# Kernel tuning notes

Hardware: AMD Instinct MI355X
Metric: run time of the kernel (lower is better)

Reference implementation:

```python
import jax, jax.numpy as jnp
import numpy as np

B2 = 8192  # 2 * batch (two SimCLR views)
D = 512    # feature_dim


def setup_inputs() -> dict:
    key = jax.random.key(0)
    k1, k2, k3 = jax.random.split(key, 3)
    feature = jax.random.normal(k1, (B2, D), dtype=jnp.float32)
    # sigma (diagonal variances) must be strictly positive: uniform in [0.5, 1.5]
    sigma_v = jax.random.uniform(k2, (B2, D), dtype=jnp.float32, minval=0.5, maxval=1.5)
    # label indexes the (B2-1) skip-self columns -> values in [0, B2-2]
    label = jax.random.randint(k3, (B2,), 0, B2 - 1)
    return {"feature": feature, "sigma_v": sigma_v, "label": label}


def reference(feature, sigma_v, label):
    n, d = feature.shape
    rows = jnp.arange(n)
    cols = jnp.arange(n - 1)
    # gather_index[b, k] = k if k < b else k + 1  (all indices except b)
    gi = cols[None, :] + (cols[None, :] >= rows[:, None]).astype(jnp.int32)  # (B2, B2-1)

    inv_s = 1.0 / sigma_v
    # weighted Mahalanobis: dist[i, j] = sum_d (x_i - x_j)^2 / sigma_j, expanded to GEMMs
    t1 = (feature * feature) @ inv_s.T                 # sum_d x_i^2 / sigma_j
    t2 = feature @ (feature * inv_s).T                 # sum_d x_i x_j / sigma_j
    t3 = jnp.sum(feature * feature * inv_s, axis=1)    # sum_d x_j^2 / sigma_j
    dist = t1 - 2.0 * t2 + t3[None, :]                 # (B2, B2)

    dist_g = jnp.take_along_axis(dist, gi, axis=1)               # (B2, B2-1)
    gt = jnp.take_along_axis(dist_g, label[:, None], axis=1)     # (B2, 1)
    logit = jnp.exp(0.1 * (gt - dist_g))                         # (B2, B2-1)

    # absolute index of each row's positive sample
    pos_idx = jnp.take_along_axis(gi, label[:, None], axis=1)[:, 0]  # (B2,)
    # ratio[i, j] = prod_d sqrt(sigma_i[d] / sigma_pos(j)[d]) = exp(0.5 * (ls[i] - ls[pos(j)]))
    ls = jnp.sum(jnp.log(sigma_v), axis=1)                           # (B2,)
    ratio_g = jnp.exp(0.5 * (ls[:, None] - ls[pos_idx][gi]))         # (B2, B2-1)

    logit_mat = ratio_g * logit
    loss = jnp.mean(jnp.log(jnp.sum(logit_mat, axis=1)))
    return loss, logit_mat
```

## Files before the change

kernel.cpp:

```cpp
#include <hip/hip_runtime.h>
#include <hip/hip_bf16.h>
#include <stdint.h>

#define B2 8192
#define D  512
#define K2 1024
#define NM1 (B2 - 1)

typedef _Float16 f16;
typedef _Float16 f16x2 __attribute__((ext_vector_type(2)));
typedef _Float16 f16x8 __attribute__((ext_vector_type(8)));
typedef float    f32x4 __attribute__((ext_vector_type(4)));

__global__ __launch_bounds__(256) void prep(
    const float* __restrict__ feat, const float* __restrict__ sig,
    const int* __restrict__ label,
    f16* __restrict__ Ahat, f16* __restrict__ Bhat,
    float* __restrict__ rowc, float* __restrict__ colc2, float* __restrict__ rowsum)
{
    int i = blockIdx.x;
    int t = threadIdx.x;
    int lb = label[i];
    int p  = lb + (lb >= i ? 1 : 0);

    const float2 xv  = ((const float2*)(feat + (size_t)i * D))[t];
    const float2 sv  = ((const float2*)(sig  + (size_t)i * D))[t];
    const float2 xpv = ((const float2*)(feat + (size_t)p * D))[t];
    const float2 spv = ((const float2*)(sig  + (size_t)p * D))[t];

    float inv0 = 1.0f / sv.x, inv1 = 1.0f / sv.y;
    float x20 = xv.x * xv.x, x21 = xv.y * xv.y;

    f16* Ar = Ahat + (size_t)i * K2;
    f16* Br = Bhat + (size_t)i * K2;
    *(f16x2*)&Ar[2 * t]       = f16x2{(f16)x20, (f16)x21};
    *(f16x2*)&Ar[512 + 2 * t] = f16x2{(f16)xv.x, (f16)xv.y};
    *(f16x2*)&Br[2 * t]       = f16x2{(f16)inv0, (f16)inv1};
    *(f16x2*)&Br[512 + 2 * t] = f16x2{(f16)(-2.0f * xv.x * inv0), (f16)(-2.0f * xv.y * inv1)};

    float t3p = x20 * inv0 + x21 * inv1;
    float lsp = __logf(sv.x) + __logf(sv.y);
    float lpp = __logf(spv.x) + __logf(spv.y);
    float dx0 = xv.x - xpv.x, dx1 = xv.y - xpv.y;
    float gtp = dx0 * dx0 / spv.x + dx1 * dx1 / spv.y;

    for (int off = 32; off; off >>= 1) {
        t3p += __shfl_down(t3p, off);
        lsp += __shfl_down(lsp, off);
        lpp += __shfl_down(lpp, off);
        gtp += __shfl_down(gtp, off);
    }
    __shared__ float w0[4], w1[4], w2[4], w3[4];
    int lane = t & 63, w = t >> 6;
    if (lane == 0) { w0[w] = t3p; w1[w] = lsp; w2[w] = lpp; w3[w] = gtp; }
    __syncthreads();
    if (t == 0) {
        float t3 = w0[0] + w0[1] + w0[2] + w0[3];
        float ls = w1[0] + w1[1] + w1[2] + w1[3];
        float lp = w2[0] + w2[1] + w2[2] + w2[3];
        float gt = w3[0] + w3[1] + w3[2] + w3[3];
        rowc[i]  = 0.1f * gt + 0.5f * ls;
        colc2[i] = -0.5f * lp - 0.1f * t3;
        rowsum[i] = 0.0f;
    }
}

__global__ __launch_bounds__(256, 4) void gemm_epilogue(
    const f16* __restrict__ Ahat, const f16* __restrict__ Bhat,
    const float* __restrict__ rowc, const float* __restrict__ colc2,
    float* __restrict__ rowsum, float* __restrict__ out)
{
    __shared__ f16 As[128 * 64];
    __shared__ f16 Bs[128 * 64];
    __shared__ float rS[128], cS[128];

    int bid = blockIdx.x;
    int bn = ((bid >> 9) << 3) + (bid & 7);
    int bm = (bid >> 3) & 63;

    int t = threadIdx.x;
    int l = t & 63, w = t >> 6;
    int wm = (w & 1) * 64, wn = (w >> 1) * 64;

    int srow   = t >> 3;
    int schunk = t & 7;
    int gchunk = schunk ^ (srow & 7);
    const f16* gA = Ahat + (size_t)(bm * 128 + srow) * K2 + gchunk * 8;
    const f16* gB = Bhat + (size_t)(bn * 128 + srow) * K2 + gchunk * 8;

    f32x4 zero4 = {0.f, 0.f, 0.f, 0.f};
    f32x4 acc[4][4];
    #pragma unroll
    for (int a = 0; a < 4; ++a)
        #pragma unroll
        for (int b = 0; b < 4; ++b) acc[a][b] = zero4;

    for (int kb = 0; kb < K2; kb += 64) {
        __syncthreads();
        #pragma unroll
        for (int rd = 0; rd < 4; ++rd) {
            __builtin_amdgcn_global_load_lds(
                (const __attribute__((address_space(1))) unsigned int*)(gA + (size_t)rd * 32 * K2 + kb),
                (__attribute__((address_space(3))) unsigned int*)(&As[rd * 2048 + w * 512]),
                16, 0, 0);
            __builtin_amdgcn_global_load_lds(
                (const __attribute__((address_space(1))) unsigned int*)(gB + (size_t)rd * 32 * K2 + kb),
                (__attribute__((address_space(3))) unsigned int*)(&Bs[rd * 2048 + w * 512]),
                16, 0, 0);
        }
        __syncthreads();

        #pragma unroll
        for (int ks = 0; ks < 2; ++ks) {
            f16x8 af[4], bf[4];
            int cl = (ks * 4 + (l >> 4)) ^ (l & 7);
            #pragma unroll
            for (int mi = 0; mi < 4; ++mi) {
                int ra = wm + mi * 16 + (l & 15);
                af[mi] = *(const f16x8*)&As[ra * 64 + cl * 8];
                int rb = wn + mi * 16 + (l & 15);
                bf[mi] = *(const f16x8*)&Bs[rb * 64 + cl * 8];
            }
            #pragma unroll
            for (int mi = 0; mi < 4; ++mi)
                #pragma unroll
                for (int ni = 0; ni < 4; ++ni)
                    acc[mi][ni] = __builtin_amdgcn_mfma_f32_16x16x32_f16(
                        af[mi], bf[ni], acc[mi][ni], 0, 0, 0);
        }
    }

    if (t < 128)      rS[t]       = rowc[bm * 128 + t];
    else              cS[t - 128] = colc2[bn * 128 + (t - 128)];
    __syncthreads();

    int quad = l >> 4, lc = l & 15;
    #pragma unroll
    for (int mi = 0; mi < 4; ++mi) {
        #pragma unroll
        for (int rg = 0; rg < 4; ++rg) {
            int il = wm + mi * 16 + quad * 4 + rg;
            int i  = bm * 128 + il;
            float rc = rS[il];
            float part = 0.f;
            #pragma unroll
            for (int ni = 0; ni < 4; ++ni) {
                int jl = wn + ni * 16 + lc;
                int j  = bn * 128 + jl;
                float v = __expf(rc - 0.1f * acc[mi][ni][rg] + cS[jl]);
                if (j != i) {
                    out[1 + (size_t)i * NM1 + (j - (j > i ? 1 : 0))] = v;
                    part += v;
                }
            }
            part += __shfl_xor(part, 1);
            part += __shfl_xor(part, 2);
            part += __shfl_xor(part, 4);
            part += __shfl_xor(part, 8);
            if (lc == 0) atomicAdd(&rowsum[i], part);
        }
    }
}

__global__ __launch_bounds__(256) void loss_k(const float* __restrict__ rowsum,
                                              float* __restrict__ out)
{
    int t = threadIdx.x;
    float s = 0.f;
    for (int r = t; r < B2; r += 256) s += __logf(rowsum[r]);
    for (int off = 32; off; off >>= 1) s += __shfl_down(s, off);
    __shared__ float wv[4];
    if ((t & 63) == 0) wv[t >> 6] = s;
    __syncthreads();
    if (t == 0) out[0] = (wv[0] + wv[1] + wv[2] + wv[3]) * (1.0f / (float)B2);
}

extern "C" void kernel_launch(void* const* d_in, const int* in_sizes, int n_in,
                              void* d_out, int out_size, void* d_ws, size_t ws_size,
                              hipStream_t stream) {
    const float* feat  = (const float*)d_in[0];
    const float* sig   = (const float*)d_in[1];
    const int*   label = (const int*)d_in[2];
    float* out = (float*)d_out;

    char* ws = (char*)d_ws;
    f16* Ahat = (f16*)ws;
    f16* Bhat = (f16*)(ws + (size_t)B2 * K2 * 2);
    float* rowc   = (float*)(ws + (size_t)B2 * K2 * 4);
    float* colc2  = rowc + B2;
    float* rowsum = colc2 + B2;

    prep<<<dim3(B2), dim3(256), 0, stream>>>(feat, sig, label, Ahat, Bhat, rowc, colc2, rowsum);
    gemm_epilogue<<<dim3(4096), dim3(256), 0, stream>>>(Ahat, Bhat, rowc, colc2, rowsum, out);
    loss_k<<<dim3(1), dim3(256), 0, stream>>>(rowsum, out);
}
```

Baseline: 526.6 us.

## Use 256x256 tiles with double-buffered LDS and interleaved async loads in GEMM

Replaces the 128x128, 256-thread GEMM tile with a 256x256 tile run by 512 threads (8 waves) that double-buffers A and B in LDS. Global-to-LDS loads for the next k-slice are issued between MFMA phases, guarded by explicit barriers, waitcnt and setprio, so memory traffic overlaps compute. Block-to-tile mapping is also changed for L2 locality. This cuts operand re-reads and sync stalls, but the kernel now needs 128KB+ of LDS and one block per CU, which lowers occupancy, and the hand-written schedule is fragile.

```diff
diff --git a/kernel.cpp b/kernel.cpp
--- a/kernel.cpp
+++ b/kernel.cpp
@@ -6,6 +6,7 @@
 #define D  512
 #define K2 1024
 #define NM1 (B2 - 1)
+#define NT  16
 
 typedef _Float16 f16;
 typedef _Float16 f16x2 __attribute__((ext_vector_type(2)));
@@ -65,88 +66,202 @@
     }
 }
 
-__global__ __launch_bounds__(256, 4) void gemm_epilogue(
+
+#define GLDS16(src, dst)                                                       \
+  __builtin_amdgcn_global_load_lds(                                            \
+      (const __attribute__((address_space(1))) unsigned int*)(src),            \
+      (__attribute__((address_space(3))) unsigned int*)(dst), 16, 0, 0)
+
+#define STAGE_HALF(gbase, hrow, koff, dstbase)                                 \
+  do {                                                                         \
+    GLDS16((gbase) + (size_t)(hrow) * K2 + (koff), (dstbase) + w512);          \
+    GLDS16((gbase) + (size_t)((hrow) + 64) * K2 + (koff),                      \
+           (dstbase) + 4096 + w512);                                           \
+  } while (0)
+
+template <int VM>
+__device__ __forceinline__ void kquad(
+    const f16* Asb, const f16* Bsb,
+    f16* AsN,
+    f16* BsC,
+    const f16* gA, const f16* gB, int w512,
+    int doA, int kA, int doB, int kB,
+    int wr128, int wc64, int l15, int lhi, int l7,
+    f32x4 (&acc)[8][4])
+{
+    f16x8 bf[4][2], af[2][2];
+
+    #pragma unroll
+    for (int ni = 0; ni < 4; ++ni)
+        #pragma unroll
+        for (int ks = 0; ks < 2; ++ks)
+            bf[ni][ks] = *(const f16x8*)&Bsb[(wc64 + ni * 16 + l15) * 64 +
+                                             (((ks * 4 + lhi) ^ l7) * 8)];
+    #pragma unroll
+    for (int m = 0; m < 2; ++m)
+        #pragma unroll
+        for (int ks = 0; ks < 2; ++ks)
+            af[m][ks] = *(const f16x8*)&Asb[(wr128 + m * 16 + l15) * 64 +
+                                            (((ks * 4 + lhi) ^ l7) * 8)];
+    if (doA) { STAGE_HALF(gA, 0, kA, AsN); }
+    asm volatile("" ::: "memory");
+    __builtin_amdgcn_s_barrier();
+    asm volatile("s_waitcnt lgkmcnt(0)" ::: "memory");
+    __builtin_amdgcn_sched_barrier(0);
+    __builtin_amdgcn_s_setprio(1);
+    #pragma unroll
+    for (int m = 0; m < 2; ++m)
+        #pragma unroll
+        for (int ni = 0; ni < 4; ++ni)
+            #pragma unroll
+            for (int ks = 0; ks < 2; ++ks)
+                acc[m][ni] = __builtin_amdgcn_mfma_f32_16x16x32_f16(
+                    af[m][ks], bf[ni][ks], acc[m][ni], 0, 0, 0);
+    __builtin_amdgcn_s_setprio(0);
+    __builtin_amdgcn_s_barrier();
+
+    #pragma unroll
+    for (int m = 0; m < 2; ++m)
+        #pragma unroll
+        for (int ks = 0; ks < 2; ++ks)
+            af[m][ks] = *(const f16x8*)&Asb[(wr128 + (2 + m) * 16 + l15) * 64 +
+                                            (((ks * 4 + lhi) ^ l7) * 8)];
+    if (doA) { STAGE_HALF(gA, 128, kA, AsN + 8192); }
+    asm volatile("" ::: "memory");
+    if (doB) { STAGE_HALF(gB, 0, kB, BsC); }
+    asm volatile("" ::: "memory");
+    __builtin_amdgcn_s_barrier();
+    asm volatile("s_waitcnt lgkmcnt(0)" ::: "memory");
+    __builtin_amdgcn_sched_barrier(0);
+    __builtin_amdgcn_s_setprio(1);
+    #pragma unroll
+    for (int m = 0; m < 2; ++m)
+        #pragma unroll
+        for (int ni = 0; ni < 4; ++ni)
+            #pragma unroll
+            for (int ks = 0; ks < 2; ++ks)
+                acc[2 + m][ni] = __builtin_amdgcn_mfma_f32_16x16x32_f16(
+                    af[m][ks], bf[ni][ks], acc[2 + m][ni], 0, 0, 0);
+    __builtin_amdgcn_s_setprio(0);
+    __builtin_amdgcn_s_barrier();
+
+    #pragma unroll
+    for (int m = 0; m < 2; ++m)
+        #pragma unroll
+        for (int ks = 0; ks < 2; ++ks)
+            af[m][ks] = *(const f16x8*)&Asb[(wr128 + (4 + m) * 16 + l15) * 64 +
+                                            (((ks * 4 + lhi) ^ l7) * 8)];
+    if (doB) { STAGE_HALF(gB, 128, kB, BsC + 8192); }
+    asm volatile("" ::: "memory");
+    __builtin_amdgcn_s_barrier();
+    asm volatile("s_waitcnt lgkmcnt(0)" ::: "memory");
+    __builtin_amdgcn_sched_barrier(0);
+    __builtin_amdgcn_s_setprio(1);
+    #pragma unroll
+    for (int m = 0; m < 2; ++m)
+        #pragma unroll
+        for (int ni = 0; ni < 4; ++ni)
+            #pragma unroll
+            for (int ks = 0; ks < 2; ++ks)
+                acc[4 + m][ni] = __builtin_amdgcn_mfma_f32_16x16x32_f16(
+                    af[m][ks], bf[ni][ks], acc[4 + m][ni], 0, 0, 0);
+    __builtin_amdgcn_s_setprio(0);
+    __builtin_amdgcn_s_barrier();
+
+    #pragma unroll
+    for (int m = 0; m < 2; ++m)
+        #pragma unroll
+        for (int ks = 0; ks < 2; ++ks)
+            af[m][ks] = *(const f16x8*)&Asb[(wr128 + (6 + m) * 16 + l15) * 64 +
+                                            (((ks * 4 + lhi) ^ l7) * 8)];
+    __builtin_amdgcn_s_barrier();
+    asm volatile("s_waitcnt lgkmcnt(0)" ::: "memory");
+    __builtin_amdgcn_sched_barrier(0);
+    __builtin_amdgcn_s_setprio(1);
+    #pragma unroll
+    for (int m = 0; m < 2; ++m)
+        #pragma unroll
+        for (int ni = 0; ni < 4; ++ni)
+            #pragma unroll
+            for (int ks = 0; ks < 2; ++ks)
+                acc[6 + m][ni] = __builtin_amdgcn_mfma_f32_16x16x32_f16(
+                    af[m][ks], bf[ni][ks], acc[6 + m][ni], 0, 0, 0);
+    __builtin_amdgcn_s_setprio(0);
+    if (VM == 4) asm volatile("s_waitcnt vmcnt(4)" ::: "memory");
+    else         asm volatile("s_waitcnt vmcnt(0)" ::: "memory");
+    __builtin_amdgcn_s_barrier();
+}
+
+__global__ __launch_bounds__(512, 1) void gemm_epilogue(
     const f16* __restrict__ Ahat, const f16* __restrict__ Bhat,
     const float* __restrict__ rowc, const float* __restrict__ colc2,
     float* __restrict__ rowsum, float* __restrict__ out)
 {
-    __shared__ f16 As[128 * 64];
-    __shared__ f16 Bs[128 * 64];
-    __shared__ float rS[128], cS[128];
+    __shared__ f16 As[2][256 * 64];
+    __shared__ f16 Bs[2][256 * 64];
+    __shared__ float rS[256], cS[256];
 
     int bid = blockIdx.x;
-    int bn = ((bid >> 9) << 3) + (bid & 7);
-    int bm = (bid >> 3) & 63;
+    int rr = bid >> 3, x = bid & 7;
+    int bm = x * 4 + (rr & 3);
+    int bn = rr >> 2;
 
     int t = threadIdx.x;
     int l = t & 63, w = t >> 6;
-    int wm = (w & 1) * 64, wn = (w >> 1) * 64;
-
-    int srow   = t >> 3;
-    int schunk = t & 7;
-    int gchunk = schunk ^ (srow & 7);
-    const f16* gA = Ahat + (size_t)(bm * 128 + srow) * K2 + gchunk * 8;
-    const f16* gB = Bhat + (size_t)(bn * 128 + srow) * K2 + gchunk * 8;
-
-    f32x4 zero4 = {0.f, 0.f, 0.f, 0.f};
-    f32x4 acc[4][4];
-    #pragma unroll
-    for (int a = 0; a < 4; ++a)
-        #pragma unroll
-        for (int b = 0; b < 4; ++b) acc[a][b] = zero4;
-
-    for (int kb = 0; kb < K2; kb += 64) {
-        __syncthreads();
-        #pragma unroll
-        for (int rd = 0; rd < 4; ++rd) {
-            __builtin_amdgcn_global_load_lds(
-                (const __attribute__((address_space(1))) unsigned int*)(gA + (size_t)rd * 32 * K2 + kb),
-                (__attribute__((address_space(3))) unsigned int*)(&As[rd * 2048 + w * 512]),
-                16, 0, 0);
-            __builtin_amdgcn_global_load_lds(
-                (const __attribute__((address_space(1))) unsigned int*)(gB + (size_t)rd * 32 * K2 + kb),
-                (__attribute__((address_space(3))) unsigned int*)(&Bs[rd * 2048 + w * 512]),
-                16, 0, 0);
-        }
-        __syncthreads();
-
-        #pragma unroll
-        for (int ks = 0; ks < 2; ++ks) {
-            f16x8 af[4], bf[4];
-            int cl = (ks * 4 + (l >> 4)) ^ (l & 7);
-            #pragma unroll
-            for (int mi = 0; mi < 4; ++mi) {
-                int ra = wm + mi * 16 + (l & 15);
-                af[mi] = *(const f16x8*)&As[ra * 64 + cl * 8];
-                int rb = wn + mi * 16 + (l & 15);
-                bf[mi] = *(const f16x8*)&Bs[rb * 64 + cl * 8];
-            }
-            #pragma unroll
-            for (int mi = 0; mi < 4; ++mi)
-                #pragma unroll
-                for (int ni = 0; ni < 4; ++ni)
-                    acc[mi][ni] = __builtin_amdgcn_mfma_f32_16x16x32_f16(
-                        af[mi], bf[ni], acc[mi][ni], 0, 0, 0);
-        }
+    int wr128 = (w >> 2) * 128;
+    int wc64  = (w & 3) * 64;
+    int l15 = l & 15, lhi = l >> 4, l7 = l & 7;
+    int w512 = w * 512;
+
+    int gcs = (t & 7) ^ ((t >> 3) & 7);
+    const f16* gA = Ahat + (size_t)(bm * 256 + (t >> 3)) * K2 + gcs * 8;
+    const f16* gB = Bhat + (size_t)(bn * 256 + (t >> 3)) * K2 + gcs * 8;
+
+    if (t < 256) rS[t]       = rowc[bm * 256 + t];
+    else         cS[t - 256] = colc2[bn * 256 + (t - 256)];
+
+    STAGE_HALF(gA, 0,   0,  &As[0][0]);
+    STAGE_HALF(gA, 128, 0,  &As[0][8192]);
+    STAGE_HALF(gB, 0,   0,  &Bs[0][0]);
+    STAGE_HALF(gB, 128, 0,  &Bs[0][8192]);
+    STAGE_HALF(gB, 0,   64, &Bs[1][0]);
+    STAGE_HALF(gB, 128, 64, &Bs[1][8192]);
+    __syncthreads();
+
+    f32x4 acc[8][4];
+    #pragma unroll
+    for (int a = 0; a < 8; ++a)
+        #pragma unroll
+        for (int b = 0; b < 4; ++b) acc[a][b] = f32x4{0.f, 0.f, 0.f, 0.f};
+
+    #pragma unroll 1
+    for (int it = 0; it < 7; ++it) {
+        int T = 2 * it;
+        kquad<4>(&As[0][0], &Bs[0][0], &As[1][0], &Bs[0][0], gA, gB, w512,
+                 1, (T + 1) * 64, 1, (T + 2) * 64,
+                 wr128, wc64, l15, lhi, l7, acc);
+        kquad<4>(&As[1][0], &Bs[1][0], &As[0][0], &Bs[1][0], gA, gB, w512,
+                 1, (T + 2) * 64, 1, (T + 3) * 64,
+                 wr128, wc64, l15, lhi, l7, acc);
     }
-
-    if (t < 128)      rS[t]       = rowc[bm * 128 + t];
-    else              cS[t - 128] = colc2[bn * 128 + (t - 128)];
-    __syncthreads();
-
-    int quad = l >> 4, lc = l & 15;
-    #pragma unroll
-    for (int mi = 0; mi < 4; ++mi) {
+    kquad<0>(&As[0][0], &Bs[0][0], &As[1][0], &Bs[0][0], gA, gB, w512,
+             1, 15 * 64, 0, 0, wr128, wc64, l15, lhi, l7, acc);
+    kquad<0>(&As[1][0], &Bs[1][0], &As[0][0], &Bs[1][0], gA, gB, w512,
+             0, 0, 0, 0, wr128, wc64, l15, lhi, l7, acc);
+
+    int qd = l >> 4, lc = l & 15;
+    #pragma unroll
+    for (int mi = 0; mi < 8; ++mi) {
         #pragma unroll
         for (int rg = 0; rg < 4; ++rg) {
-            int il = wm + mi * 16 + quad * 4 + rg;
-            int i  = bm * 128 + il;
+            int il = wr128 + mi * 16 + qd * 4 + rg;
+            int i  = bm * 256 + il;
             float rc = rS[il];
             float part = 0.f;
             #pragma unroll
             for (int ni = 0; ni < 4; ++ni) {
-                int jl = wn + ni * 16 + lc;
-                int j  = bn * 128 + jl;
+                int jl = wc64 + ni * 16 + lc;
+                int j  = bn * 256 + jl;
                 float v = __expf(rc - 0.1f * acc[mi][ni][rg] + cS[jl]);
                 if (j != i) {
                     out[1 + (size_t)i * NM1 + (j - (j > i ? 1 : 0))] = v;
@@ -191,6 +306,6 @@
     float* rowsum = colc2 + B2;
 
     prep<<<dim3(B2), dim3(256), 0, stream>>>(feat, sig, label, Ahat, Bhat, rowc, colc2, rowsum);
-    gemm_epilogue<<<dim3(4096), dim3(256), 0, stream>>>(Ahat, Bhat, rowc, colc2, rowsum, out);
+    gemm_epilogue<<<dim3(1024), dim3(512), 0, stream>>>(Ahat, Bhat, rowc, colc2, rowsum, out);
     loss_k<<<dim3(1), dim3(256), 0, stream>>>(rowsum, out);
 }
```

Result: faster. 463.1 us (-12.1%).
